# Performance work log

Measured on AMD Instinct MI355X. Metric: run time of the kernel, lower is better.

## Reference

```python
import jax, jax.numpy as jnp
import numpy as np

D_MODEL, N_LEVELS, N_HEADS, N_POINTS = 256, 4, 8, 4
DH = D_MODEL // N_HEADS
SPATIAL = np.array([[92, 92], [46, 46], [23, 23], [12, 12]], dtype=np.int64)
LEVEL_START = np.concatenate([[0], np.cumsum(SPATIAL[:, 0] * SPATIAL[:, 1])[:-1]]).astype(np.int64)
LEN_IN = int((SPATIAL[:, 0] * SPATIAL[:, 1]).sum())  # 11253
B, Q = 2, LEN_IN


def _radial_bias():
    # Matches FlashDeformAttnTorch._reset_parameters sampling_offsets bias init.
    thetas = np.arange(N_HEADS, dtype=np.float32) * (2.0 * np.pi / N_HEADS)
    grid = np.stack([np.cos(thetas), np.sin(thetas)], -1)  # (G,2)
    grid = grid / np.abs(grid).max(-1, keepdims=True)
    grid = np.tile(grid[:, None, None, :], (1, N_LEVELS, N_POINTS, 1)).copy()
    for i in range(N_POINTS):
        grid[:, :, i, :] *= i + 1
    return jnp.asarray(grid.reshape(-1), dtype=jnp.float32)


def setup_inputs() -> dict:
    key = jax.random.key(0)
    ks = jax.random.split(key, 10)
    s = 1.0 / np.sqrt(D_MODEL)
    return {
        "query": jax.random.normal(ks[0], (B, Q, D_MODEL), jnp.float32),
        "reference_points": jax.random.uniform(ks[1], (B, Q, N_LEVELS, 2), jnp.float32),
        "input_flatten": jax.random.normal(ks[2], (B, LEN_IN, D_MODEL), jnp.float32),
        "spatial_shapes": SPATIAL,
        "level_start_index": LEVEL_START,
        "W_off": jax.random.normal(ks[3], (D_MODEL, N_HEADS * N_LEVELS * N_POINTS * 2), jnp.float32) * 0.01,
        "b_off": _radial_bias(),
        "W_attn": jax.random.normal(ks[4], (D_MODEL, N_HEADS * N_LEVELS * N_POINTS), jnp.float32) * 0.01,
        "b_attn": jnp.zeros((N_HEADS * N_LEVELS * N_POINTS,), jnp.float32),
        "W_val": jax.random.normal(ks[5], (D_MODEL, D_MODEL), jnp.float32) * s,
        "b_val": jnp.zeros((D_MODEL,), jnp.float32),
        "W_out": jax.random.normal(ks[6], (D_MODEL, D_MODEL), jnp.float32) * s,
        "b_out": jnp.zeros((D_MODEL,), jnp.float32),
    }


def _forward(query, reference_points, input_flatten, W_off, b_off, W_attn, b_attn,
             W_val, b_val, W_out, b_out, spatial_shapes, level_start_index):
    Bn, Qn, _ = query.shape
    G, L, K, Dh = N_HEADS, N_LEVELS, N_POINTS, DH
    ss = np.asarray(spatial_shapes)
    lsi = np.asarray(level_start_index)

    value = (input_flatten @ W_val + b_val).reshape(Bn, -1, G, Dh)
    offsets = (query @ W_off + b_off).reshape(Bn, Qn, G, L, K, 2)
    logits = (query @ W_attn + b_attn).reshape(Bn, Qn, G, L * K)
    attn = jax.nn.softmax(logits, axis=-1).reshape(Bn, Qn, G, L, K)

    # normalizer stacks (W, H) per level
    normalizer = jnp.asarray(np.stack([ss[:, 1], ss[:, 0]], -1).astype(np.float32))
    loc = reference_points[:, :, None, :, None, :] + offsets / normalizer[None, None, None, :, None, :]
    # loc: (B, Q, G, L, K, 2) with (..., 0)=x, (..., 1)=y in [0,1]

    out = jnp.zeros((Bn, Qn, G, Dh), value.dtype)
    for lvl in range(L):
        H, W = int(ss[lvl, 0]), int(ss[lvl, 1])
        start = int(lsi[lvl])
        vlev = value[:, start:start + H * W].transpose(0, 2, 1, 3)  # (B, G, H*W, Dh)
        h_im = loc[:, :, :, lvl, :, 1] * H - 0.5  # (B, Q, G, K)
        w_im = loc[:, :, :, lvl, :, 0] * W - 0.5
        h0 = jnp.floor(h_im); w0 = jnp.floor(w_im)
        lh = h_im - h0; lw = w_im - w0
        hh = 1.0 - lh; hw = 1.0 - lw
        h0i = h0.astype(jnp.int32); w0i = w0.astype(jnp.int32)

        def corner(hi, wi, vlev=vlev, H=H, W=W):
            m = (hi >= 0) & (hi < H) & (wi >= 0) & (wi < W)
            idx = jnp.clip(hi, 0, H - 1) * W + jnp.clip(wi, 0, W - 1)  # (B,Q,G,K)
            idx_bg = idx.transpose(0, 2, 1, 3).reshape(Bn, G, Qn * K)
            g = jax.vmap(jax.vmap(lambda v, i: v[i]))(vlev, idx_bg)  # (B,G,Q*K,Dh)
            g = g.reshape(Bn, G, Qn, K, Dh).transpose(0, 2, 1, 3, 4)  # (B,Q,G,K,Dh)
            return g * m.transpose(0, 1, 2, 3)[..., None].astype(g.dtype)

        v1 = corner(h0i, w0i)
        v2 = corner(h0i, w0i + 1)
        v3 = corner(h0i + 1, w0i)
        v4 = corner(h0i + 1, w0i + 1)
        sampled = (v1 * (hh * hw)[..., None] + v2 * (hh * lw)[..., None]
                   + v3 * (lh * hw)[..., None] + v4 * (lh * lw)[..., None])
        valid = (h_im > -1) & (w_im > -1) & (h_im < H) & (w_im < W)
        sampled = sampled * valid[..., None].astype(sampled.dtype)
        out = out + (sampled * attn[:, :, :, lvl, :, None]).sum(axis=3)

    out = out.reshape(Bn, Qn, G * Dh)
    return out @ W_out + b_out


def reference(query, reference_points, input_flatten, spatial_shapes, level_start_index,
              W_off, b_off, W_attn, b_attn, W_val, b_val, W_out, b_out):
    return _forward(query, reference_points, input_flatten, W_off, b_off, W_attn, b_attn,
                    W_val, b_val, W_out, b_out, spatial_shapes, level_start_index)
```

## Files before the change

kernel.cpp:

```cpp
#include <hip/hip_runtime.h>
#include <math.h>

#define NQ      11253
#define MTOT    22506
#define MPAD    22528
#define LEN_IN  11253

typedef unsigned short u16;
typedef u16   u16x8 __attribute__((ext_vector_type(8)));
typedef float f32x4 __attribute__((ext_vector_type(4)));

__device__ __forceinline__ u16 f2bf(float x) {
    unsigned u = __float_as_uint(x);
    return (u16)((u + 0x7fffu + ((u >> 16) & 1u)) >> 16);
}
__device__ __forceinline__ float bf2f(u16 h) {
    return __uint_as_float(((unsigned)h) << 16);
}
__device__ __forceinline__ void MFMA(f32x4& d, u16x8 a, u16x8 b) {
    asm("v_mfma_f32_16x16x32_bf16 %0, %1, %2, %0" : "+v"(d) : "v"(a), "v"(b));
}
__device__ __forceinline__ void glds16(const void* g, void* l) {
    __builtin_amdgcn_global_load_lds(
        (const __attribute__((address_space(1))) unsigned int*)g,
        (__attribute__((address_space(3))) unsigned int*)l, 16, 0, 0);
}

__global__ __launch_bounds__(256) void prep(
    const float* __restrict__ inputf,
    const float* __restrict__ Wv, const float* __restrict__ Wo,
    const float* __restrict__ Wa, const float* __restrict__ Wu,
    u16* __restrict__ ih, u16* __restrict__ wvh, u16* __restrict__ wolh,
    u16* __restrict__ wuh)
{
    const int t = threadIdx.x;
    if (blockIdx.y == 0) {
        const int row = blockIdx.x * 8 + (t >> 5);
        const int col = (t & 31) * 8;
        float4 v0 = make_float4(0.f, 0.f, 0.f, 0.f), v1 = v0;
        if (row < MTOT) {
            v0 = *(const float4*)&inputf[(size_t)row * 256 + col];
            v1 = *(const float4*)&inputf[(size_t)row * 256 + col + 4];
        }
        const float v[8] = {v0.x, v0.y, v0.z, v0.w, v1.x, v1.y, v1.z, v1.w};
        u16x8 hi;
#pragma unroll
        for (int j = 0; j < 8; ++j) hi[j] = f2bf(v[j]);
        *(u16x8*)&ih[(size_t)row * 256 + col] = hi;
    } else {
        const int k = blockIdx.x;
        if (k >= 256) return;
        wvh[t * 256 + k] = f2bf(Wv[k * 256 + t]);
        wuh[t * 256 + k] = f2bf(Wu[k * 256 + t]);
        wolh[t * 256 + k] = f2bf(Wo[k * 256 + t]);
        if (t < 128) wolh[(256 + t) * 256 + k] = f2bf(Wa[k * 128 + t]);
    }
}

template <int N, int NT, int ASRC, int OUTMODE>
__global__ __launch_bounds__(256) void gemm2(
    const float* __restrict__ Af32,
    const u16* __restrict__ Ah, const u16* __restrict__ Al,
    const u16* __restrict__ Bh, const u16* __restrict__ Bl,
    const float* __restrict__ bias0, const float* __restrict__ bias1,
    float* __restrict__ Cf, u16* __restrict__ Cb)
{
    __shared__ __align__(16) u16 AS0[128 * 64];
    __shared__ __align__(16) u16 BS0[128 * 64];
    __shared__ __align__(16) u16 AS1[(NT == 3) ? 128 * 64 : 8];
    __shared__ __align__(16) u16 BS1[(NT == 3) ? 128 * 64 : 8];

    const int tid = threadIdx.x;
    const int l = tid & 63, wid = tid >> 6;
    const int wr = wid >> 1, wc = wid & 1;
    const int lr = l & 15;
    const int bm = blockIdx.x * 128, bn = blockIdx.y * 128;

    f32x4 acc[4][4];
#pragma unroll
    for (int i = 0; i < 4; ++i)
#pragma unroll
        for (int j = 0; j < 4; ++j) acc[i][j] = (f32x4)0.f;

    for (int k0 = 0; k0 < 256; k0 += 64) {
        if constexpr (ASRC == 0) {
#pragma unroll
            for (int j = 0; j < 4; ++j) {
                const int ld = wid * 4 + j;
                const int r  = ld * 8 + (l >> 3);
                const int gs = (l & 7) ^ (l >> 3);
                const size_t gi = (size_t)(bm + r) * 256 + k0 + gs * 8;
                glds16(Ah + gi, &AS0[ld * 512]);
                if constexpr (NT == 3) glds16(Al + gi, &AS1[ld * 512]);
            }
        } else {
            const int r = tid >> 1, h = tid & 1;
            const bool ok = (bm + r) < MTOT;
            const float* src = &Af32[(size_t)(bm + r) * 256 + k0 + h * 32];
            float4 f[8];
#pragma unroll
            for (int c = 0; c < 4; ++c) {
                f[2 * c]     = ok ? *(const float4*)(src + c * 8)     : make_float4(0.f,0.f,0.f,0.f);
                f[2 * c + 1] = ok ? *(const float4*)(src + c * 8 + 4) : make_float4(0.f,0.f,0.f,0.f);
            }
#pragma unroll
            for (int c = 0; c < 4; ++c) {
                const int s = h * 4 + c;
                const float* p = (const float*)&f[2 * c];
                u16x8 hv;
#pragma unroll
                for (int j = 0; j < 8; ++j) hv[j] = f2bf(p[j]);
                *(u16x8*)&AS0[r * 64 + ((s ^ (r & 7)) * 8)] = hv;
            }
        }
#pragma unroll
        for (int j = 0; j < 4; ++j) {
            const int ld = wid * 4 + j;
            const int rn = ld * 8 + (l >> 3);
            const int gs = (l & 7) ^ (l >> 3);
            const size_t gi = (size_t)(bn + rn) * 256 + k0 + gs * 8;
            glds16(Bh + gi, &BS0[ld * 512]);
            if constexpr (NT == 3) glds16(Bl + gi, &BS1[ld * 512]);
        }
        __syncthreads();

#pragma unroll
        for (int kk = 0; kk < 2; ++kk) {
            const int ks = kk * 4 + (l >> 4);
            u16x8 a0[4], b0[4], a1[4], b1[4];
#pragma unroll
            for (int t4 = 0; t4 < 4; ++t4) {
                const int ra = wr * 64 + t4 * 16 + lr;
                const int rb = wc * 64 + t4 * 16 + lr;
                const int sa = (ks ^ (ra & 7)) * 8;
                const int sb = (ks ^ (rb & 7)) * 8;
                a0[t4] = *(const u16x8*)&AS0[ra * 64 + sa];
                b0[t4] = *(const u16x8*)&BS0[rb * 64 + sb];
                if constexpr (NT == 3) {
                    a1[t4] = *(const u16x8*)&AS1[ra * 64 + sa];
                    b1[t4] = *(const u16x8*)&BS1[rb * 64 + sb];
                }
            }
#pragma unroll
            for (int mt = 0; mt < 4; ++mt)
#pragma unroll
                for (int nt = 0; nt < 4; ++nt) {
                    MFMA(acc[mt][nt], a0[mt], b0[nt]);
                    if constexpr (NT == 3) {
                        MFMA(acc[mt][nt], a0[mt], b1[nt]);
                        MFMA(acc[mt][nt], a1[mt], b0[nt]);
                    }
                }
        }
        __syncthreads();
    }

    asm volatile("s_nop 7\n\ts_nop 7");

#pragma unroll
    for (int mt = 0; mt < 4; ++mt)
#pragma unroll
        for (int j = 0; j < 4; ++j) {
            const int m = bm + wr * 64 + mt * 16 + (l >> 4) * 4 + j;
            if (m >= MTOT) continue;
#pragma unroll
            for (int nt = 0; nt < 4; ++nt) {
                const int n = bn + wc * 64 + nt * 16 + lr;
                const float val = acc[mt][nt][j];
                if constexpr (OUTMODE == 0) {
                    Cf[(size_t)m * 256 + n] = val + bias0[n];
                } else if constexpr (OUTMODE == 1) {
                    const int bi = (m >= LEN_IN) ? 1 : 0;
                    const int pix = m - bi * LEN_IN;
                    Cb[((size_t)((bi << 3) | (n >> 5)) * LEN_IN + pix) * 32 + (n & 31)]
                        = f2bf(val + bias0[n]);
                } else {
                    if (n < 256) Cf[(size_t)m * 256 + n] = val + bias0[n];
                    else ((float*)Cb)[(size_t)m * 128 + (n - 256)] = val + bias1[n - 256];
                }
            }
        }
}

__global__ __launch_bounds__(256) void deform_sample(
    const u16* __restrict__ valbf, const float* __restrict__ offsets,
    const float* __restrict__ logits, const float* __restrict__ refp,
    u16* __restrict__ inner)
{
    const int tid = threadIdx.x;
    const int qi = blockIdx.x * 8 + (tid >> 5);
    if (qi >= MTOT) return;
    const int lq = tid & 31;
    const int g = lq >> 2, d8 = (lq & 3) * 8;
    const int b = (qi >= NQ) ? 1 : 0;

    const float* lg  = logits  + (size_t)qi * 128 + g * 16;
    const float* off = offsets + (size_t)qi * 256 + g * 32;
    const float* ref = refp    + (size_t)qi * 8;
    const u16* vbase = valbf + ((size_t)(b * 8 + g) * LEN_IN) * 32 + d8;

    float w[16];
    float mx = -1e30f;
#pragma unroll
    for (int i = 0; i < 16; ++i) { w[i] = lg[i]; mx = fmaxf(mx, w[i]); }
    float s = 0.f;
#pragma unroll
    for (int i = 0; i < 16; ++i) { w[i] = __expf(w[i] - mx); s += w[i]; }
    const float inv = 1.f / s;

    constexpr int Hs[4] = {92, 46, 23, 12};
    constexpr int Ss[4] = {0, 8464, 10580, 11109};

    float acc[8];
#pragma unroll
    for (int j = 0; j < 8; ++j) acc[j] = 0.f;

#pragma unroll
    for (int l = 0; l < 4; ++l) {
        const int Hn = Hs[l];
        const float Hf = (float)Hn;
        const float rx = ref[l * 2 + 0];
        const float ry = ref[l * 2 + 1];
        const u16* vlev = vbase + (size_t)Ss[l] * 32;

        uint4 cv[16];
        float cw[16];
#pragma unroll
        for (int k = 0; k < 4; ++k) {
            const float ox = off[(l * 4 + k) * 2 + 0];
            const float oy = off[(l * 4 + k) * 2 + 1];
            const float x = (rx + ox / Hf) * Hf - 0.5f;
            const float y = (ry + oy / Hf) * Hf - 0.5f;
            float aw = w[l * 4 + k];
            if (!(y > -1.f && x > -1.f && y < Hf && x < Hf)) aw = 0.f;
            const float h0f = floorf(y), w0f = floorf(x);
            const float lh = y - h0f, lw = x - w0f;
            const float hh = 1.f - lh, hw = 1.f - lw;
            const int h0 = (int)h0f, w0 = (int)w0f;
            const int base = h0 * Hn + w0;
            const bool hv0 = (unsigned)h0 < (unsigned)Hn;
            const bool hv1 = (unsigned)(h0 + 1) < (unsigned)Hn;
            const bool wv0 = (unsigned)w0 < (unsigned)Hn;
            const bool wv1 = (unsigned)(w0 + 1) < (unsigned)Hn;
            const bool v00 = hv0 && wv0, v01 = hv0 && wv1;
            const bool v10 = hv1 && wv0, v11 = hv1 && wv1;
            cw[k * 4 + 0] = v00 ? hh * hw * aw : 0.f;
            cw[k * 4 + 1] = v01 ? hh * lw * aw : 0.f;
            cw[k * 4 + 2] = v10 ? lh * hw * aw : 0.f;
            cw[k * 4 + 3] = v11 ? lh * lw * aw : 0.f;
            cv[k * 4 + 0] = *(const uint4*)(vlev + (size_t)(v00 ? base : 0) * 32);
            cv[k * 4 + 1] = *(const uint4*)(vlev + (size_t)(v01 ? base + 1 : 0) * 32);
            cv[k * 4 + 2] = *(const uint4*)(vlev + (size_t)(v10 ? base + Hn : 0) * 32);
            cv[k * 4 + 3] = *(const uint4*)(vlev + (size_t)(v11 ? base + Hn + 1 : 0) * 32);
        }
#pragma unroll
        for (int i = 0; i < 16; ++i) {
            const float c_ = cw[i];
            const uint4 v = cv[i];
            acc[0] += __uint_as_float(v.x << 16) * c_;
            acc[1] += __uint_as_float(v.x & 0xffff0000u) * c_;
            acc[2] += __uint_as_float(v.y << 16) * c_;
            acc[3] += __uint_as_float(v.y & 0xffff0000u) * c_;
            acc[4] += __uint_as_float(v.z << 16) * c_;
            acc[5] += __uint_as_float(v.z & 0xffff0000u) * c_;
            acc[6] += __uint_as_float(v.w << 16) * c_;
            acc[7] += __uint_as_float(v.w & 0xffff0000u) * c_;
        }
    }

    u16x8 hv;
#pragma unroll
    for (int j = 0; j < 8; ++j) hv[j] = f2bf(acc[j] * inv);
    *(u16x8*)&inner[(size_t)qi * 256 + g * 32 + d8] = hv;
}

extern "C" void kernel_launch(void* const* d_in, const int* in_sizes, int n_in,
                              void* d_out, int out_size, void* d_ws, size_t ws_size,
                              hipStream_t stream)
{
    const float* query  = (const float*)d_in[0];
    const float* refp   = (const float*)d_in[1];
    const float* inputf = (const float*)d_in[2];
    const float* W_off  = (const float*)d_in[5];
    const float* b_off  = (const float*)d_in[6];
    const float* W_att  = (const float*)d_in[7];
    const float* b_att  = (const float*)d_in[8];
    const float* W_val  = (const float*)d_in[9];
    const float* b_val  = (const float*)d_in[10];
    const float* W_out  = (const float*)d_in[11];
    const float* b_out  = (const float*)d_in[12];
    float* out = (float*)d_out;

    char* ws = (char*)d_ws;
    size_t o = 0;
    float* offsets = (float*)(ws + o); o += (size_t)MTOT * 256 * 4;
    float* logits  = (float*)(ws + o); o += (size_t)MTOT * 128 * 4;
    u16*   valbf   = (u16*)  (ws + o); o += (size_t)MTOT * 256 * 2;
    u16*   inner_h = (u16*)  (ws + o); o += (size_t)MPAD * 256 * 2;
    u16*   wvh     = (u16*)  (ws + o); o += 256 * 256 * 2;
    u16*   wolh    = (u16*)  (ws + o); o += 384 * 256 * 2;
    u16*   wuh     = (u16*)  (ws + o); o += 256 * 256 * 2;
    u16*   ih      = inner_h;

    dim3 blk(256);

    hipLaunchKernelGGL(prep, dim3(2816, 2), blk, 0, stream,
                       inputf, W_val, W_off, W_att, W_out, ih, wvh, wolh, wuh);

    hipLaunchKernelGGL((gemm2<256, 1, 0, 1>), dim3(176, 2), blk, 0, stream,
                       (const float*)nullptr, ih, (const u16*)nullptr, wvh, (const u16*)nullptr,
                       b_val, (const float*)nullptr, (float*)nullptr, valbf);
    hipLaunchKernelGGL((gemm2<384, 1, 1, 2>), dim3(176, 3), blk, 0, stream,
                       query, (const u16*)nullptr, (const u16*)nullptr, wolh, (const u16*)nullptr,
                       b_off, b_att, offsets, (u16*)logits);

    hipLaunchKernelGGL(deform_sample, dim3((MTOT + 7) / 8), blk, 0, stream,
                       valbf, offsets, logits, refp, inner_h);

    hipLaunchKernelGGL((gemm2<256, 1, 0, 0>), dim3(176, 2), blk, 0, stream,
                       (const float*)nullptr, inner_h, (const u16*)nullptr, wuh, (const u16*)nullptr,
                       b_out, (const float*)nullptr, out, (u16*)nullptr);
}
```

Baseline: 206.6 us.

## Fuse value and offset/attention projections into one GEMM launch, drop input pre-conversion

The separate pass that converted the whole input_flatten to bf16 is removed. The value projection now reads fp32 input and converts it while staging into LDS. The value GEMM and the offset/logit GEMM are merged into a single launch with a 5-column grid, where blockIdx.y picks the A source, the weight slice and the output mode. This saves a full read and write of the input tensor plus one kernel launch, and gives a larger grid to fill the GPU. In exchange, the value GEMM now does register-side conversion and loses the direct global-to-LDS loads for A.

```diff
diff --git a/kernel.cpp b/kernel.cpp
--- a/kernel.cpp
+++ b/kernel.cpp
@@ -26,49 +26,130 @@
         (__attribute__((address_space(3))) unsigned int*)l, 16, 0, 0);
 }
 
-__global__ __launch_bounds__(256) void prep(
-    const float* __restrict__ inputf,
+__global__ __launch_bounds__(256) void prep_w(
     const float* __restrict__ Wv, const float* __restrict__ Wo,
     const float* __restrict__ Wa, const float* __restrict__ Wu,
-    u16* __restrict__ ih, u16* __restrict__ wvh, u16* __restrict__ wolh,
-    u16* __restrict__ wuh)
-{
+    u16* __restrict__ wvh, u16* __restrict__ wolh, u16* __restrict__ wuh)
+{
+    const int k = blockIdx.x;
     const int t = threadIdx.x;
-    if (blockIdx.y == 0) {
-        const int row = blockIdx.x * 8 + (t >> 5);
-        const int col = (t & 31) * 8;
-        float4 v0 = make_float4(0.f, 0.f, 0.f, 0.f), v1 = v0;
-        if (row < MTOT) {
-            v0 = *(const float4*)&inputf[(size_t)row * 256 + col];
-            v1 = *(const float4*)&inputf[(size_t)row * 256 + col + 4];
-        }
-        const float v[8] = {v0.x, v0.y, v0.z, v0.w, v1.x, v1.y, v1.z, v1.w};
-        u16x8 hi;
-#pragma unroll
-        for (int j = 0; j < 8; ++j) hi[j] = f2bf(v[j]);
-        *(u16x8*)&ih[(size_t)row * 256 + col] = hi;
-    } else {
-        const int k = blockIdx.x;
-        if (k >= 256) return;
-        wvh[t * 256 + k] = f2bf(Wv[k * 256 + t]);
-        wuh[t * 256 + k] = f2bf(Wu[k * 256 + t]);
-        wolh[t * 256 + k] = f2bf(Wo[k * 256 + t]);
-        if (t < 128) wolh[(256 + t) * 256 + k] = f2bf(Wa[k * 128 + t]);
-    }
-}
-
-template <int N, int NT, int ASRC, int OUTMODE>
-__global__ __launch_bounds__(256) void gemm2(
-    const float* __restrict__ Af32,
-    const u16* __restrict__ Ah, const u16* __restrict__ Al,
-    const u16* __restrict__ Bh, const u16* __restrict__ Bl,
-    const float* __restrict__ bias0, const float* __restrict__ bias1,
-    float* __restrict__ Cf, u16* __restrict__ Cb)
+    wvh[t * 256 + k] = f2bf(Wv[k * 256 + t]);
+    wuh[t * 256 + k] = f2bf(Wu[k * 256 + t]);
+    wolh[t * 256 + k] = f2bf(Wo[k * 256 + t]);
+    if (t < 128) wolh[(256 + t) * 256 + k] = f2bf(Wa[k * 128 + t]);
+}
+
+__global__ __launch_bounds__(256) void gemm_s1(
+    const float* __restrict__ inputf, const float* __restrict__ query,
+    const u16* __restrict__ wvh, const u16* __restrict__ wolh,
+    const float* __restrict__ bias_v, const float* __restrict__ bias_o,
+    const float* __restrict__ bias_a,
+    float* __restrict__ offsets, float* __restrict__ logits,
+    u16* __restrict__ valbf)
 {
     __shared__ __align__(16) u16 AS0[128 * 64];
     __shared__ __align__(16) u16 BS0[128 * 64];
-    __shared__ __align__(16) u16 AS1[(NT == 3) ? 128 * 64 : 8];
-    __shared__ __align__(16) u16 BS1[(NT == 3) ? 128 * 64 : 8];
+
+    const int tid = threadIdx.x;
+    const int l = tid & 63, wid = tid >> 6;
+    const int wr = wid >> 1, wc = wid & 1;
+    const int lr = l & 15;
+    const int bm = blockIdx.x * 128;
+    const int ny = blockIdx.y;
+
+    const float* A = (ny < 2) ? inputf : query;
+    const u16*   B = (ny < 2) ? (wvh + ny * 128 * 256)
+                              : (wolh + (ny - 2) * 128 * 256);
+
+    f32x4 acc[4][4];
+#pragma unroll
+    for (int i = 0; i < 4; ++i)
+#pragma unroll
+        for (int j = 0; j < 4; ++j) acc[i][j] = (f32x4)0.f;
+
+    for (int k0 = 0; k0 < 256; k0 += 64) {
+        {
+            const int r = tid >> 1, h = tid & 1;
+            const bool ok = (bm + r) < MTOT;
+            const float* src = &A[(size_t)(bm + r) * 256 + k0 + h * 32];
+            float4 f[8];
+#pragma unroll
+            for (int c = 0; c < 4; ++c) {
+                f[2 * c]     = ok ? *(const float4*)(src + c * 8)     : make_float4(0.f,0.f,0.f,0.f);
+                f[2 * c + 1] = ok ? *(const float4*)(src + c * 8 + 4) : make_float4(0.f,0.f,0.f,0.f);
+            }
+#pragma unroll
+            for (int c = 0; c < 4; ++c) {
+                const int s = h * 4 + c;
+                const float* p = (const float*)&f[2 * c];
+                u16x8 hv;
+#pragma unroll
+                for (int j = 0; j < 8; ++j) hv[j] = f2bf(p[j]);
+                *(u16x8*)&AS0[r * 64 + ((s ^ (r & 7)) * 8)] = hv;
+            }
+        }
+#pragma unroll
+        for (int j = 0; j < 4; ++j) {
+            const int ld = wid * 4 + j;
+            const int rn = ld * 8 + (l >> 3);
+            const int gs = (l & 7) ^ (l >> 3);
+            glds16(B + (size_t)rn * 256 + k0 + gs * 8, &BS0[ld * 512]);
+        }
+        __syncthreads();
+
+#pragma unroll
+        for (int kk = 0; kk < 2; ++kk) {
+            const int ks = kk * 4 + (l >> 4);
+            u16x8 a0[4], b0[4];
+#pragma unroll
+            for (int t4 = 0; t4 < 4; ++t4) {
+                const int ra = wr * 64 + t4 * 16 + lr;
+                const int rb = wc * 64 + t4 * 16 + lr;
+                a0[t4] = *(const u16x8*)&AS0[ra * 64 + ((ks ^ (ra & 7)) * 8)];
+                b0[t4] = *(const u16x8*)&BS0[rb * 64 + ((ks ^ (rb & 7)) * 8)];
+            }
+#pragma unroll
+            for (int mt = 0; mt < 4; ++mt)
+#pragma unroll
+                for (int nt = 0; nt < 4; ++nt)
+                    MFMA(acc[mt][nt], a0[mt], b0[nt]);
+        }
+        __syncthreads();
+    }
+
+    asm volatile("s_nop 7\n\ts_nop 7");
+
+#pragma unroll
+    for (int mt = 0; mt < 4; ++mt)
+#pragma unroll
+        for (int j = 0; j < 4; ++j) {
+            const int m = bm + wr * 64 + mt * 16 + (l >> 4) * 4 + j;
+            if (m >= MTOT) continue;
+#pragma unroll
+            for (int nt = 0; nt < 4; ++nt) {
+                const int nl = wc * 64 + nt * 16 + lr;
+                const float val = acc[mt][nt][j];
+                if (ny < 2) {
+                    const int n = ny * 128 + nl;
+                    const int bi = (m >= LEN_IN) ? 1 : 0;
+                    const int pix = m - bi * LEN_IN;
+                    valbf[((size_t)((bi << 3) | (n >> 5)) * LEN_IN + pix) * 32 + (n & 31)]
+                        = f2bf(val + bias_v[n]);
+                } else {
+                    const int n = (ny - 2) * 128 + nl;
+                    if (n < 256) offsets[(size_t)m * 256 + n] = val + bias_o[n];
+                    else logits[(size_t)m * 128 + (n - 256)] = val + bias_a[n - 256];
+                }
+            }
+        }
+}
+
+__global__ __launch_bounds__(256) void gemm_out(
+    const u16* __restrict__ Ah, const u16* __restrict__ Bh,
+    const float* __restrict__ bias0, float* __restrict__ Cf)
+{
+    __shared__ __align__(16) u16 AS0[128 * 64];
+    __shared__ __align__(16) u16 BS0[128 * 64];
 
     const int tid = threadIdx.x;
     const int l = tid & 63, wid = tid >> 6;
@@ -83,74 +164,32 @@
         for (int j = 0; j < 4; ++j) acc[i][j] = (f32x4)0.f;
 
     for (int k0 = 0; k0 < 256; k0 += 64) {
-        if constexpr (ASRC == 0) {
-#pragma unroll
-            for (int j = 0; j < 4; ++j) {
-                const int ld = wid * 4 + j;
-                const int r  = ld * 8 + (l >> 3);
-                const int gs = (l & 7) ^ (l >> 3);
-                const size_t gi = (size_t)(bm + r) * 256 + k0 + gs * 8;
-                glds16(Ah + gi, &AS0[ld * 512]);
-                if constexpr (NT == 3) glds16(Al + gi, &AS1[ld * 512]);
-            }
-        } else {
-            const int r = tid >> 1, h = tid & 1;
-            const bool ok = (bm + r) < MTOT;
-            const float* src = &Af32[(size_t)(bm + r) * 256 + k0 + h * 32];
-            float4 f[8];
-#pragma unroll
-            for (int c = 0; c < 4; ++c) {
-                f[2 * c]     = ok ? *(const float4*)(src + c * 8)     : make_float4(0.f,0.f,0.f,0.f);
-                f[2 * c + 1] = ok ? *(const float4*)(src + c * 8 + 4) : make_float4(0.f,0.f,0.f,0.f);
-            }
-#pragma unroll
-            for (int c = 0; c < 4; ++c) {
-                const int s = h * 4 + c;
-                const float* p = (const float*)&f[2 * c];
-                u16x8 hv;
-#pragma unroll
-                for (int j = 0; j < 8; ++j) hv[j] = f2bf(p[j]);
-                *(u16x8*)&AS0[r * 64 + ((s ^ (r & 7)) * 8)] = hv;
-            }
-        }
 #pragma unroll
         for (int j = 0; j < 4; ++j) {
             const int ld = wid * 4 + j;
-            const int rn = ld * 8 + (l >> 3);
+            const int r  = ld * 8 + (l >> 3);
             const int gs = (l & 7) ^ (l >> 3);
-            const size_t gi = (size_t)(bn + rn) * 256 + k0 + gs * 8;
-            glds16(Bh + gi, &BS0[ld * 512]);
-            if constexpr (NT == 3) glds16(Bl + gi, &BS1[ld * 512]);
+            glds16(Ah + (size_t)(bm + r) * 256 + k0 + gs * 8, &AS0[ld * 512]);
+            glds16(Bh + (size_t)(bn + r) * 256 + k0 + gs * 8, &BS0[ld * 512]);
         }
         __syncthreads();
 
 #pragma unroll
         for (int kk = 0; kk < 2; ++kk) {
             const int ks = kk * 4 + (l >> 4);
-            u16x8 a0[4], b0[4], a1[4], b1[4];
+            u16x8 a0[4], b0[4];
 #pragma unroll
             for (int t4 = 0; t4 < 4; ++t4) {
                 const int ra = wr * 64 + t4 * 16 + lr;
                 const int rb = wc * 64 + t4 * 16 + lr;
-                const int sa = (ks ^ (ra & 7)) * 8;
-                const int sb = (ks ^ (rb & 7)) * 8;
-                a0[t4] = *(const u16x8*)&AS0[ra * 64 + sa];
-                b0[t4] = *(const u16x8*)&BS0[rb * 64 + sb];
-                if constexpr (NT == 3) {
-                    a1[t4] = *(const u16x8*)&AS1[ra * 64 + sa];
-                    b1[t4] = *(const u16x8*)&BS1[rb * 64 + sb];
-                }
+                a0[t4] = *(const u16x8*)&AS0[ra * 64 + ((ks ^ (ra & 7)) * 8)];
+                b0[t4] = *(const u16x8*)&BS0[rb * 64 + ((ks ^ (rb & 7)) * 8)];
             }
 #pragma unroll
             for (int mt = 0; mt < 4; ++mt)
 #pragma unroll
-                for (int nt = 0; nt < 4; ++nt) {
+                for (int nt = 0; nt < 4; ++nt)
                     MFMA(acc[mt][nt], a0[mt], b0[nt]);
-                    if constexpr (NT == 3) {
-                        MFMA(acc[mt][nt], a0[mt], b1[nt]);
-                        MFMA(acc[mt][nt], a1[mt], b0[nt]);
-                    }
-                }
         }
         __syncthreads();
     }
@@ -166,18 +205,7 @@
 #pragma unroll
             for (int nt = 0; nt < 4; ++nt) {
                 const int n = bn + wc * 64 + nt * 16 + lr;
-                const float val = acc[mt][nt][j];
-                if constexpr (OUTMODE == 0) {
-                    Cf[(size_t)m * 256 + n] = val + bias0[n];
-                } else if constexpr (OUTMODE == 1) {
-                    const int bi = (m >= LEN_IN) ? 1 : 0;
-                    const int pix = m - bi * LEN_IN;
-                    Cb[((size_t)((bi << 3) | (n >> 5)) * LEN_IN + pix) * 32 + (n & 31)]
-                        = f2bf(val + bias0[n]);
-                } else {
-                    if (n < 256) Cf[(size_t)m * 256 + n] = val + bias0[n];
-                    else ((float*)Cb)[(size_t)m * 128 + (n - 256)] = val + bias1[n - 256];
-                }
+                Cf[(size_t)m * 256 + n] = acc[mt][nt][j] + bias0[n];
             }
         }
 }
@@ -296,28 +324,23 @@
     float* offsets = (float*)(ws + o); o += (size_t)MTOT * 256 * 4;
     float* logits  = (float*)(ws + o); o += (size_t)MTOT * 128 * 4;
     u16*   valbf   = (u16*)  (ws + o); o += (size_t)MTOT * 256 * 2;
-    u16*   inner_h = (u16*)  (ws + o); o += (size_t)MPAD * 256 * 2;
+    u16*   inner   = (u16*)  (ws + o); o += (size_t)MPAD * 256 * 2;
     u16*   wvh     = (u16*)  (ws + o); o += 256 * 256 * 2;
     u16*   wolh    = (u16*)  (ws + o); o += 384 * 256 * 2;
     u16*   wuh     = (u16*)  (ws + o); o += 256 * 256 * 2;
-    u16*   ih      = inner_h;
 
     dim3 blk(256);
 
-    hipLaunchKernelGGL(prep, dim3(2816, 2), blk, 0, stream,
-                       inputf, W_val, W_off, W_att, W_out, ih, wvh, wolh, wuh);
-
-    hipLaunchKernelGGL((gemm2<256, 1, 0, 1>), dim3(176, 2), blk, 0, stream,
-                       (const float*)nullptr, ih, (const u16*)nullptr, wvh, (const u16*)nullptr,
-                       b_val, (const float*)nullptr, (float*)nullptr, valbf);
-    hipLaunchKernelGGL((gemm2<384, 1, 1, 2>), dim3(176, 3), blk, 0, stream,
-                       query, (const u16*)nullptr, (const u16*)nullptr, wolh, (const u16*)nullptr,
-                       b_off, b_att, offsets, (u16*)logits);
+    hipLaunchKernelGGL(prep_w, dim3(256), blk, 0, stream,
+                       W_val, W_off, W_att, W_out, wvh, wolh, wuh);
+
+    hipLaunchKernelGGL(gemm_s1, dim3(176, 5), blk, 0, stream,
+                       inputf, query, wvh, wolh, b_val, b_off, b_att,
+                       offsets, logits, valbf);
 
     hipLaunchKernelGGL(deform_sample, dim3((MTOT + 7) / 8), blk, 0, stream,
-                       valbf, offsets, logits, refp, inner_h);
-
-    hipLaunchKernelGGL((gemm2<256, 1, 0, 0>), dim3(176, 2), blk, 0, stream,
-                       (const float*)nullptr, inner_h, (const u16*)nullptr, wuh, (const u16*)nullptr,
-                       b_out, (const float*)nullptr, out, (u16*)nullptr);
-}
+                       valbf, offsets, logits, refp, inner);
+
+    hipLaunchKernelGGL(gemm_out, dim3(176, 2), blk, 0, stream,
+                       inner, wuh, b_out, out);
+}
```

After: 209.6 us. About the same (+1.4%).
